# Performance work log

Hardware: AMD Instinct MI355X
Metric: run time of the kernel (lower is better)

The kernel has to match this reference:

```python
import jax, jax.numpy as jnp
import numpy as np
import math

ALPHA, BETA = 0.0, 0.1  # MarketRelation defaults


def setup_inputs() -> dict:
    key = jax.random.key(0)
    ks = jax.random.split(key, 15)
    n, T, d, K, C = 1024, 8, 64, 8, 64
    h = d  # hidden = (2*infeat)//2 = infeat
    s = 0.1
    u = jax.random.uniform(ks[13], (n, n, K), jnp.float32, 1e-6, 1.0 - 1e-6)
    return {
        "x":   jax.random.normal(ks[0], (n, T, d), jnp.float32),
        "Ind": jax.random.uniform(ks[1], (n, n), jnp.float32),
        "Loc": jax.random.uniform(ks[2], (n, n), jnp.float32),
        "a":   jax.random.normal(ks[3], (T, 1), jnp.float32),
        "W1m": jax.random.normal(ks[4], (2 * d, h), jnp.float32) * s,
        "b1m": jax.random.normal(ks[5], (h,), jnp.float32) * s,
        "W2m": jax.random.normal(ks[6], (h, 1), jnp.float32) * s,
        "b2m": jax.random.normal(ks[7], (1,), jnp.float32) * s,
        "W1s": jax.random.normal(ks[8], (2 * d, h), jnp.float32) * s,
        "b1s": jax.random.normal(ks[9], (h,), jnp.float32) * s,
        "W2s": jax.random.normal(ks[10], (h, K), jnp.float32) * s,
        "b2s": jax.random.normal(ks[11], (K,), jnp.float32) * s,
        "E":   jax.random.normal(ks[12], (K, n, C), jnp.float32) * s,
        "g":   -jnp.log(-jnp.log(u)),  # Gumbel(0,1) noise for gumbel_softmax
    }


def reference(x, Ind, Loc, a, W1m, b1m, W2m, b2m, W1s, b1s, W2s, b2s, E, g):
    n, T, d = x.shape
    # --- MarketRelation ---
    # fc1(concat(x_j, x_k)) == x_j @ W1m[:d] + x_k @ W1m[d:] + b1m (same math,
    # avoids materializing the N x N x 2d concat tensor)
    W1a, W1b = W1m[:d], W1m[d:]
    a_soft = jax.nn.softmax(a, axis=0)  # [T,1]
    A_mkt = jnp.zeros((n, n), x.dtype)
    for i in range(T):
        xi = x[:, i, :]                      # [n,d]
        hA = xi @ W1a                        # [n,h]
        hB = xi @ W1b                        # [n,h]
        hmat = jax.nn.relu(hA[:, None, :] + hB[None, :, :] + b1m)  # [n,n,h]
        adj = jax.nn.relu(hmat @ W2m + b2m)[..., 0]                # [n,n]
        factor = 1.0 + ALPHA * math.exp(-BETA * (T - i - 1))
        A_mkt = A_mkt + adj * (a_soft[i, 0] * factor)
    # --- NobsRelation (on last timestep) ---
    xl = x[:, -1, :]
    Ws1a, Ws1b = W1s[:d], W1s[d:]
    hs = jax.nn.relu((xl @ Ws1a)[:, None, :] + (xl @ Ws1b)[None, :, :] + b1s)
    logits = jax.nn.relu(hs @ W2s + b2s)          # [n,n,K]
    y = jax.nn.softmax(logits + g, axis=-1)       # gumbel_softmax, tau=1, soft
    D = jnp.einsum('knc,kmc->nmk', E, E)          # stack of E_k E_k^T, [n,n,K]
    A_nobs = jnp.sum(D * y, axis=-1)              # [n,n]
    return jnp.stack([Ind, Loc, A_mkt, A_nobs])   # [4,n,n]
```

## Files before the change

kernel.cpp:

```cpp
#include <hip/hip_runtime.h>

typedef unsigned short USH;
typedef float v2f __attribute__((ext_vector_type(2)));

__device__ __forceinline__ float bf2f(USH u) {
    return __uint_as_float(((unsigned int)u) << 16);
}
__device__ __forceinline__ float lo16(unsigned int u) { return __uint_as_float(u << 16); }
__device__ __forceinline__ float hi16(unsigned int u) { return __uint_as_float(u & 0xFFFF0000u); }
__device__ __forceinline__ USH f2bf(float f) {
    unsigned int i = __float_as_uint(f);
    i += 0x7FFFu + ((i >> 16) & 1u);
    return (USH)(i >> 16);
}
__device__ __forceinline__ v2f relu2(v2f s) {
    return __builtin_elementwise_max(s, (v2f)(0.0f));
}

__device__ __forceinline__ float ldf(const void* p, long idx, int bf) {
    return bf ? bf2f(((const USH*)p)[idx]) : ((const float*)p)[idx];
}
__device__ __forceinline__ void ld4(const void* p, long idx, int bf, float o[4]) {
    if (bf) {
        ushort4 u = *(const ushort4*)((const USH*)p + idx);
        o[0] = bf2f(u.x); o[1] = bf2f(u.y); o[2] = bf2f(u.z); o[3] = bf2f(u.w);
    } else {
        float4 v = *(const float4*)((const float*)p + idx);
        o[0] = v.x; o[1] = v.y; o[2] = v.z; o[3] = v.w;
    }
}

__device__ __forceinline__ int detect_bf(const void* ind) {
    const uint4* p = (const uint4*)ind;
    unsigned o = 0;
    #pragma unroll
    for (int i = 0; i < 8; ++i) { uint4 v = p[i]; o |= v.x | v.y | v.z | v.w; }
    return (o & 0x8000u) == 0;
}

__global__ __launch_bounds__(256) void k_pre_d(
    const void* __restrict__ x,
    const void* __restrict__ W1m,
    const void* __restrict__ b1m,
    const void* __restrict__ W1s,
    const void* __restrict__ b1s,
    const void* __restrict__ E,
    const void* __restrict__ IndDet,
    USH* __restrict__ hA, USH* __restrict__ hBb,
    USH* __restrict__ hsA, USH* __restrict__ hsBb,
    USH* __restrict__ D)
{
    __shared__ float smem[8192];
    float* sA = smem;
    float* sB = smem + 4096;
    const int bf = detect_bf(IndDet);
    const int tid = threadIdx.x;
    const int bid = blockIdx.x;
    const int tx = tid & 15, ty = tid >> 4;

    if (bid < 2048) {
        const int mb = (bid & 15) * 64, nb = ((bid >> 4) & 15) * 64, k = bid >> 8;
        const long ek = (long)k * 65536;
        {
            const int r_l = tid >> 2, cq = tid & 3;
            const long bn = ek + (long)(nb + r_l) * 64 + cq * 16;
            const long bm = ek + (long)(mb + r_l) * 64 + cq * 16;
            #pragma unroll
            for (int j = 0; j < 4; ++j) {
                const int c0 = cq * 16 + j * 4;
                float o[4];
                ld4(E, bn + j * 4, bf, o);
                #pragma unroll
                for (int e = 0; e < 4; ++e) sA[(c0 + e) * 64 + r_l] = o[e];
                ld4(E, bm + j * 4, bf, o);
                #pragma unroll
                for (int e = 0; e < 4; ++e) sB[(c0 + e) * 64 + r_l] = o[e];
            }
        }
        __syncthreads();
        const int m0 = tx * 4, n0 = ty * 4;
        float acc[4][4] = {};
        #pragma unroll 8
        for (int c = 0; c < 64; ++c) {
            const float4 an = *(const float4*)&sA[c * 64 + n0];
            const float4 am = *(const float4*)&sB[c * 64 + m0];
            const float aa[4] = {an.x, an.y, an.z, an.w};
            const float bb[4] = {am.x, am.y, am.z, am.w};
            #pragma unroll
            for (int ni = 0; ni < 4; ++ni)
                #pragma unroll
                for (int mi = 0; mi < 4; ++mi)
                    acc[ni][mi] += aa[ni] * bb[mi];
        }
        #pragma unroll
        for (int ni = 0; ni < 4; ++ni) {
            ushort4 o;
            o.x = f2bf(acc[ni][0]); o.y = f2bf(acc[ni][1]);
            o.z = f2bf(acc[ni][2]); o.w = f2bf(acc[ni][3]);
            *(ushort4*)&D[(long)k * 1048576 + (long)(nb + n0 + ni) * 1024 + mb + m0] = o;
        }
    } else {
        const int bid2 = bid - 2048;
        const int nbase = (bid2 & 15) * 64;
        const int by = bid2 >> 4;
        int t, rb;
        const void* Wsrc;
        const void* bias;
        USH* dst;
        if (by < 8)        { t = by;     rb = 0;  Wsrc = W1m; bias = nullptr; dst = hA + by * 65536; }
        else if (by < 16)  { t = by - 8; rb = 64; Wsrc = W1m; bias = b1m;     dst = hBb + (by - 8) * 65536; }
        else if (by == 16) { t = 7;      rb = 0;  Wsrc = W1s; bias = nullptr; dst = hsA; }
        else               { t = 7;      rb = 64; Wsrc = W1s; bias = b1s;     dst = hsBb; }

        {
            const int n_l = tid >> 2, dq = tid & 3;
            const long base = (long)(nbase + n_l) * 512 + t * 64 + dq * 16;
            #pragma unroll
            for (int j = 0; j < 4; ++j) {
                float o[4]; ld4(x, base + j * 4, bf, o);
                const int d0 = dq * 16 + j * 4;
                #pragma unroll
                for (int e = 0; e < 4; ++e) sA[(d0 + e) * 64 + n_l] = o[e];
            }
        }
        {
            const int d_l = tid >> 2, cq = tid & 3;
            const long base = (long)(rb + d_l) * 64 + cq * 16;
            #pragma unroll
            for (int j = 0; j < 4; ++j) {
                float o[4]; ld4(Wsrc, base + j * 4, bf, o);
                const int c0 = cq * 16 + j * 4;
                #pragma unroll
                for (int e = 0; e < 4; ++e) sB[d_l * 64 + c0 + e] = o[e];
            }
        }
        __syncthreads();

        const int c0 = tx * 4, nq = ty * 4;
        float acc[4][4] = {};
        #pragma unroll 16
        for (int d = 0; d < 64; ++d) {
            const float4 xa = *(const float4*)&sA[d * 64 + nq];
            const float4 wv = *(const float4*)&sB[d * 64 + c0];
            const float aa[4] = {xa.x, xa.y, xa.z, xa.w};
            const float ww[4] = {wv.x, wv.y, wv.z, wv.w};
            #pragma unroll
            for (int ci = 0; ci < 4; ++ci)
                #pragma unroll
                for (int ni = 0; ni < 4; ++ni)
                    acc[ci][ni] += ww[ci] * aa[ni];
        }
        #pragma unroll
        for (int ci = 0; ci < 4; ++ci) {
            const float bb = bias ? ldf(bias, c0 + ci, bf) : 0.0f;
            ushort4 o;
            o.x = f2bf(acc[ci][0] + bb); o.y = f2bf(acc[ci][1] + bb);
            o.z = f2bf(acc[ci][2] + bb); o.w = f2bf(acc[ci][3] + bb);
            *(ushort4*)&dst[(c0 + ci) * 1024 + nbase + nq] = o;
        }
    }
}

__global__ __launch_bounds__(256, 4) void k_main(
    const USH* __restrict__ hA, const USH* __restrict__ hBb,
    const USH* __restrict__ hsA, const USH* __restrict__ hsBb,
    const USH* __restrict__ Dm,
    const void* __restrict__ Ind, const void* __restrict__ Loc,
    const void* __restrict__ a, const void* __restrict__ W2m,
    const void* __restrict__ b2m, const void* __restrict__ W2s,
    const void* __restrict__ b2s, const void* __restrict__ g,
    void* __restrict__ out)
{
    __shared__ float As[2][64 * 32];
    __shared__ float Bs[2][64 * 32];
    __shared__ float w2s_l[64 * 8];
    __shared__ float w2m_l[64];
    __shared__ float asoft_l[8];

    const int bf = detect_bf(Ind);
    const int tid = threadIdx.x;
    const int mb = blockIdx.x * 32, nb = blockIdx.y * 32;
    const int tx = tid & 15, ty = tid >> 4;
    const int m0 = tx * 2, n0 = ty * 2;

    if (tid < 64) w2m_l[tid] = ldf(W2m, tid, bf);
    if (tid >= 64 && tid < 192) {
        const int q = tid - 64;
        float o[4]; ld4(W2s, q * 4, bf, o);
        #pragma unroll
        for (int e = 0; e < 4; ++e) w2s_l[q * 4 + e] = o[e];
    }
    if (tid < 8) {
        float av[8], mx = -1e30f, s = 0.0f;
        #pragma unroll
        for (int k = 0; k < 8; ++k) { av[k] = ldf(a, k, bf); mx = fmaxf(mx, av[k]); }
        #pragma unroll
        for (int k = 0; k < 8; ++k) s += __expf(av[k] - mx);
        asoft_l[tid] = __expf(av[tid] - mx) / s;
    }
    const float b2m_f = ldf(b2m, 0, bf);

    const int offA = (tid >> 2) * 1024 + nb + (tid & 3) * 8;
    const int offB = (tid >> 2) * 1024 + mb + (tid & 3) * 8;
    const int ldsOff = tid * 8;

    {
        const uint4 pa = *(const uint4*)(hA + offA);
        const uint4 pb = *(const uint4*)(hBb + offB);
        float4 fa0, fa1, fb0, fb1;
        fa0.x = lo16(pa.x); fa0.y = hi16(pa.x); fa0.z = lo16(pa.y); fa0.w = hi16(pa.y);
        fa1.x = lo16(pa.z); fa1.y = hi16(pa.z); fa1.z = lo16(pa.w); fa1.w = hi16(pa.w);
        fb0.x = lo16(pb.x); fb0.y = hi16(pb.x); fb0.z = lo16(pb.y); fb0.w = hi16(pb.y);
        fb1.x = lo16(pb.z); fb1.y = hi16(pb.z); fb1.z = lo16(pb.w); fb1.w = hi16(pb.w);
        *(float4*)&As[0][ldsOff] = fa0; *(float4*)&As[0][ldsOff + 4] = fa1;
        *(float4*)&Bs[0][ldsOff] = fb0; *(float4*)&Bs[0][ldsOff + 4] = fb1;
    }
    __syncthreads();

    v2f amk2[2] = {(v2f)(0.0f), (v2f)(0.0f)};

    for (int t = 0; t < 8; ++t) {
        const int cur = t & 1, nxt = cur ^ 1;
        const USH* srcA = (t < 7) ? (hA + (t + 1) * 65536) : hsA;
        const USH* srcB = (t < 7) ? (hBb + (t + 1) * 65536) : hsBb;
        const uint4 pa = *(const uint4*)(srcA + offA);
        const uint4 pb = *(const uint4*)(srcB + offB);

        v2f acc2[2] = {(v2f)(0.0f), (v2f)(0.0f)};
        #pragma unroll
        for (int c4 = 0; c4 < 16; ++c4) {
            const float4 wq = *(const float4*)&w2m_l[c4 * 4];
            const float ww[4] = {wq.x, wq.y, wq.z, wq.w};
            #pragma unroll
            for (int j = 0; j < 4; ++j) {
                const int c = c4 * 4 + j;
                const v2f aa = *(const v2f*)&As[cur][(c << 5) + n0];
                const v2f bb = *(const v2f*)&Bs[cur][(c << 5) + m0];
                const v2f wv = (v2f)(ww[j]);
                const v2f s0 = relu2((v2f)(aa.x) + bb);
                const v2f s1 = relu2((v2f)(aa.y) + bb);
                acc2[0] = __builtin_elementwise_fma(s0, wv, acc2[0]);
                acc2[1] = __builtin_elementwise_fma(s1, wv, acc2[1]);
            }
        }
        const v2f asv = (v2f)(asoft_l[t]);
        const v2f b2v = (v2f)(b2m_f);
        amk2[0] = __builtin_elementwise_fma(relu2(acc2[0] + b2v), asv, amk2[0]);
        amk2[1] = __builtin_elementwise_fma(relu2(acc2[1] + b2v), asv, amk2[1]);

        float4 f0, f1;
        f0.x = lo16(pa.x); f0.y = hi16(pa.x); f0.z = lo16(pa.y); f0.w = hi16(pa.y);
        f1.x = lo16(pa.z); f1.y = hi16(pa.z); f1.z = lo16(pa.w); f1.w = hi16(pa.w);
        *(float4*)&As[nxt][ldsOff] = f0; *(float4*)&As[nxt][ldsOff + 4] = f1;
        f0.x = lo16(pb.x); f0.y = hi16(pb.x); f0.z = lo16(pb.y); f0.w = hi16(pb.y);
        f1.x = lo16(pb.z); f1.y = hi16(pb.z); f1.z = lo16(pb.w); f1.w = hi16(pb.w);
        *(float4*)&Bs[nxt][ldsOff] = f0; *(float4*)&Bs[nxt][ldsOff + 4] = f1;
        __syncthreads();
    }

    v2f lgp[2][8];
    #pragma unroll
    for (int i = 0; i < 2; ++i)
        #pragma unroll
        for (int k = 0; k < 8; ++k) lgp[i][k] = (v2f)(0.0f);

    #pragma unroll 4
    for (int c = 0; c < 64; ++c) {
        const v2f aa = *(const v2f*)&As[0][(c << 5) + n0];
        const v2f bb = *(const v2f*)&Bs[0][(c << 5) + m0];
        const v2f z0 = relu2((v2f)(aa.x) + bb);
        const v2f z1 = relu2((v2f)(aa.y) + bb);
        const float4 wa = *(const float4*)&w2s_l[c << 3];
        const float4 wb = *(const float4*)&w2s_l[(c << 3) + 4];
        const float wk[8] = {wa.x, wa.y, wa.z, wa.w, wb.x, wb.y, wb.z, wb.w};
        #pragma unroll
        for (int k = 0; k < 8; ++k) {
            const v2f wkv = (v2f)(wk[k]);
            lgp[0][k] = __builtin_elementwise_fma(z0, wkv, lgp[0][k]);
            lgp[1][k] = __builtin_elementwise_fma(z1, wkv, lgp[1][k]);
        }
    }

    float b2s_f[8];
    #pragma unroll
    for (int k = 0; k < 8; ++k) b2s_f[k] = ldf(b2s, k, bf);

    #pragma unroll
    for (int i = 0; i < 2; ++i) {
        const long rowoff = (long)(nb + n0 + i) * 1024 + mb + m0;
        float gv[16];
        ld4(g, rowoff * 8 + 0, bf, gv + 0);
        ld4(g, rowoff * 8 + 4, bf, gv + 4);
        ld4(g, rowoff * 8 + 8, bf, gv + 8);
        ld4(g, rowoff * 8 + 12, bf, gv + 12);

        float s0 = 0.0f, s1 = 0.0f, d0 = 0.0f, d1 = 0.0f;
        #pragma unroll
        for (int k = 0; k < 8; ++k) {
            const v2f lr = relu2(lgp[i][k] + (v2f)(b2s_f[k]));
            const float e0 = __expf(lr.x + gv[k]);
            const float e1 = __expf(lr.y + gv[8 + k]);
            s0 += e0; s1 += e1;
            const ushort2 dv = *(const ushort2*)&Dm[((long)k << 20) + rowoff];
            d0 += bf2f(dv.x) * e0;
            d1 += bf2f(dv.y) * e1;
        }

        if (bf) {
            USH* o = (USH*)out;
            *(ushort2*)&o[rowoff] = *(const ushort2*)&((const USH*)Ind)[rowoff];
            *(ushort2*)&o[1048576 + rowoff] = *(const ushort2*)&((const USH*)Loc)[rowoff];
            ushort2 o2; o2.x = f2bf(amk2[i].x); o2.y = f2bf(amk2[i].y);
            *(ushort2*)&o[2 * 1048576 + rowoff] = o2;
            ushort2 o3; o3.x = f2bf(d0 / s0); o3.y = f2bf(d1 / s1);
            *(ushort2*)&o[3 * 1048576 + rowoff] = o3;
        } else {
            float* o = (float*)out;
            *(float2*)&o[rowoff] = *(const float2*)&((const float*)Ind)[rowoff];
            *(float2*)&o[1048576 + rowoff] = *(const float2*)&((const float*)Loc)[rowoff];
            float2 o2; o2.x = amk2[i].x; o2.y = amk2[i].y;
            *(float2*)&o[2 * 1048576 + rowoff] = o2;
            float2 o3; o3.x = d0 / s0; o3.y = d1 / s1;
            *(float2*)&o[3 * 1048576 + rowoff] = o3;
        }
    }
}

extern "C" void kernel_launch(void* const* d_in, const int* in_sizes, int n_in,
                              void* d_out, int out_size, void* d_ws, size_t ws_size,
                              hipStream_t stream) {
    const void* x   = d_in[0];
    const void* Ind = d_in[1];
    const void* Loc = d_in[2];
    const void* a   = d_in[3];
    const void* W1m = d_in[4];
    const void* b1m = d_in[5];
    const void* W2m = d_in[6];
    const void* b2m = d_in[7];
    const void* W1s = d_in[8];
    const void* b1s = d_in[9];
    const void* W2s = d_in[10];
    const void* b2s = d_in[11];
    const void* E   = d_in[12];
    const void* g   = d_in[13];

    USH* ws   = (USH*)d_ws;
    USH* hA   = ws;
    USH* hBb  = hA + 524288;
    USH* hsA  = hBb + 524288;
    USH* hsBb = hsA + 65536;
    USH* Dm   = hsBb + 65536;

    k_pre_d<<<dim3(2336), 256, 0, stream>>>(x, W1m, b1m, W1s, b1s, E, Ind,
                                            hA, hBb, hsA, hsBb, Dm);
    k_main<<<dim3(32, 32), 256, 0, stream>>>(hA, hBb, hsA, hsBb, Dm,
                                             Ind, Loc, a, W2m, b2m, W2s, b2s,
                                             g, d_out);
}
```

Before: 187.1 us.

## Store hidden projections in fp32 and enlarge main-kernel tile to 64x32

The precompute kernel now writes the hA/hB/hsA/hsB projections as fp32 instead of bf16. This removes the bf16 unpack work in the main kernel and may change numerics slightly. The main kernel's n-tile doubles to 64 rows, so each thread computes 4x2 outputs and each B element loaded into LDS is reused more. In exchange it uses more LDS, more registers (launch bounds drop to 2 blocks per CU), a bigger workspace, and launches half as many blocks.

```diff
diff --git a/kernel.cpp b/kernel.cpp
--- a/kernel.cpp
+++ b/kernel.cpp
@@ -46,8 +46,8 @@
     const void* __restrict__ b1s,
     const void* __restrict__ E,
     const void* __restrict__ IndDet,
-    USH* __restrict__ hA, USH* __restrict__ hBb,
-    USH* __restrict__ hsA, USH* __restrict__ hsBb,
+    float* __restrict__ hA, float* __restrict__ hBb,
+    float* __restrict__ hsA, float* __restrict__ hsBb,
     USH* __restrict__ D)
 {
     __shared__ float smem[8192];
@@ -106,7 +106,7 @@
         int t, rb;
         const void* Wsrc;
         const void* bias;
-        USH* dst;
+        float* dst;
         if (by < 8)        { t = by;     rb = 0;  Wsrc = W1m; bias = nullptr; dst = hA + by * 65536; }
         else if (by < 16)  { t = by - 8; rb = 64; Wsrc = W1m; bias = b1m;     dst = hBb + (by - 8) * 65536; }
         else if (by == 16) { t = 7;      rb = 0;  Wsrc = W1s; bias = nullptr; dst = hsA; }
@@ -153,17 +153,17 @@
         #pragma unroll
         for (int ci = 0; ci < 4; ++ci) {
             const float bb = bias ? ldf(bias, c0 + ci, bf) : 0.0f;
-            ushort4 o;
-            o.x = f2bf(acc[ci][0] + bb); o.y = f2bf(acc[ci][1] + bb);
-            o.z = f2bf(acc[ci][2] + bb); o.w = f2bf(acc[ci][3] + bb);
-            *(ushort4*)&dst[(c0 + ci) * 1024 + nbase + nq] = o;
-        }
-    }
-}
-
-__global__ __launch_bounds__(256, 4) void k_main(
-    const USH* __restrict__ hA, const USH* __restrict__ hBb,
-    const USH* __restrict__ hsA, const USH* __restrict__ hsBb,
+            float4 v;
+            v.x = acc[ci][0] + bb; v.y = acc[ci][1] + bb;
+            v.z = acc[ci][2] + bb; v.w = acc[ci][3] + bb;
+            *(float4*)&dst[(c0 + ci) * 1024 + nbase + nq] = v;
+        }
+    }
+}
+
+__global__ __launch_bounds__(256, 2) void k_main(
+    const float* __restrict__ hA, const float* __restrict__ hBb,
+    const float* __restrict__ hsA, const float* __restrict__ hsBb,
     const USH* __restrict__ Dm,
     const void* __restrict__ Ind, const void* __restrict__ Loc,
     const void* __restrict__ a, const void* __restrict__ W2m,
@@ -171,7 +171,7 @@
     const void* __restrict__ b2s, const void* __restrict__ g,
     void* __restrict__ out)
 {
-    __shared__ float As[2][64 * 32];
+    __shared__ float As[2][64 * 64];
     __shared__ float Bs[2][64 * 32];
     __shared__ float w2s_l[64 * 8];
     __shared__ float w2m_l[64];
@@ -179,9 +179,9 @@
 
     const int bf = detect_bf(Ind);
     const int tid = threadIdx.x;
-    const int mb = blockIdx.x * 32, nb = blockIdx.y * 32;
+    const int mb = blockIdx.x * 32, nb = blockIdx.y * 64;
     const int tx = tid & 15, ty = tid >> 4;
-    const int m0 = tx * 2, n0 = ty * 2;
+    const int m0 = tx * 2, n0 = ty * 4;
 
     if (tid < 64) w2m_l[tid] = ldf(W2m, tid, bf);
     if (tid >= 64 && tid < 192) {
@@ -200,33 +200,39 @@
     }
     const float b2m_f = ldf(b2m, 0, bf);
 
-    const int offA = (tid >> 2) * 1024 + nb + (tid & 3) * 8;
-    const int offB = (tid >> 2) * 1024 + mb + (tid & 3) * 8;
-    const int ldsOff = tid * 8;
-
-    {
-        const uint4 pa = *(const uint4*)(hA + offA);
-        const uint4 pb = *(const uint4*)(hBb + offB);
-        float4 fa0, fa1, fb0, fb1;
-        fa0.x = lo16(pa.x); fa0.y = hi16(pa.x); fa0.z = lo16(pa.y); fa0.w = hi16(pa.y);
-        fa1.x = lo16(pa.z); fa1.y = hi16(pa.z); fa1.z = lo16(pa.w); fa1.w = hi16(pa.w);
-        fb0.x = lo16(pb.x); fb0.y = hi16(pb.x); fb0.z = lo16(pb.y); fb0.w = hi16(pb.y);
-        fb1.x = lo16(pb.z); fb1.y = hi16(pb.z); fb1.z = lo16(pb.w); fb1.w = hi16(pb.w);
-        *(float4*)&As[0][ldsOff] = fa0; *(float4*)&As[0][ldsOff + 4] = fa1;
-        *(float4*)&Bs[0][ldsOff] = fb0; *(float4*)&Bs[0][ldsOff + 4] = fb1;
-    }
+    int gA[4], gB[2];
+    #pragma unroll
+    for (int j = 0; j < 4; ++j) {
+        const int ch = tid + j * 256;
+        gA[j] = (ch >> 4) * 1024 + nb + (ch & 15) * 4;
+    }
+    #pragma unroll
+    for (int j = 0; j < 2; ++j) {
+        const int ch = tid + j * 256;
+        gB[j] = (ch >> 3) * 1024 + mb + (ch & 7) * 4;
+    }
+
+    #pragma unroll
+    for (int j = 0; j < 4; ++j)
+        *(float4*)&As[0][(tid + j * 256) * 4] = *(const float4*)&hA[gA[j]];
+    #pragma unroll
+    for (int j = 0; j < 2; ++j)
+        *(float4*)&Bs[0][(tid + j * 256) * 4] = *(const float4*)&hBb[gB[j]];
     __syncthreads();
 
-    v2f amk2[2] = {(v2f)(0.0f), (v2f)(0.0f)};
+    v2f amk2[4] = {(v2f)(0.0f), (v2f)(0.0f), (v2f)(0.0f), (v2f)(0.0f)};
 
     for (int t = 0; t < 8; ++t) {
         const int cur = t & 1, nxt = cur ^ 1;
-        const USH* srcA = (t < 7) ? (hA + (t + 1) * 65536) : hsA;
-        const USH* srcB = (t < 7) ? (hBb + (t + 1) * 65536) : hsBb;
-        const uint4 pa = *(const uint4*)(srcA + offA);
-        const uint4 pb = *(const uint4*)(srcB + offB);
-
-        v2f acc2[2] = {(v2f)(0.0f), (v2f)(0.0f)};
+        const float* srcA = (t < 7) ? (hA + (t + 1) * 65536) : hsA;
+        const float* srcB = (t < 7) ? (hBb + (t + 1) * 65536) : hsBb;
+        float4 pa[4], pb[2];
+        #pragma unroll
+        for (int j = 0; j < 4; ++j) pa[j] = *(const float4*)&srcA[gA[j]];
+        #pragma unroll
+        for (int j = 0; j < 2; ++j) pb[j] = *(const float4*)&srcB[gB[j]];
+
+        v2f acc2[4] = {(v2f)(0.0f), (v2f)(0.0f), (v2f)(0.0f), (v2f)(0.0f)};
         #pragma unroll
         for (int c4 = 0; c4 < 16; ++c4) {
             const float4 wq = *(const float4*)&w2m_l[c4 * 4];
@@ -234,50 +240,55 @@
             #pragma unroll
             for (int j = 0; j < 4; ++j) {
                 const int c = c4 * 4 + j;
-                const v2f aa = *(const v2f*)&As[cur][(c << 5) + n0];
+                const float4 aa = *(const float4*)&As[cur][(c << 6) + n0];
                 const v2f bb = *(const v2f*)&Bs[cur][(c << 5) + m0];
                 const v2f wv = (v2f)(ww[j]);
-                const v2f s0 = relu2((v2f)(aa.x) + bb);
-                const v2f s1 = relu2((v2f)(aa.y) + bb);
-                acc2[0] = __builtin_elementwise_fma(s0, wv, acc2[0]);
-                acc2[1] = __builtin_elementwise_fma(s1, wv, acc2[1]);
+                const float an[4] = {aa.x, aa.y, aa.z, aa.w};
+                #pragma unroll
+                for (int i = 0; i < 4; ++i) {
+                    const v2f s = relu2((v2f)(an[i]) + bb);
+                    acc2[i] = __builtin_elementwise_fma(s, wv, acc2[i]);
+                }
             }
         }
         const v2f asv = (v2f)(asoft_l[t]);
         const v2f b2v = (v2f)(b2m_f);
-        amk2[0] = __builtin_elementwise_fma(relu2(acc2[0] + b2v), asv, amk2[0]);
-        amk2[1] = __builtin_elementwise_fma(relu2(acc2[1] + b2v), asv, amk2[1]);
-
-        float4 f0, f1;
-        f0.x = lo16(pa.x); f0.y = hi16(pa.x); f0.z = lo16(pa.y); f0.w = hi16(pa.y);
-        f1.x = lo16(pa.z); f1.y = hi16(pa.z); f1.z = lo16(pa.w); f1.w = hi16(pa.w);
-        *(float4*)&As[nxt][ldsOff] = f0; *(float4*)&As[nxt][ldsOff + 4] = f1;
-        f0.x = lo16(pb.x); f0.y = hi16(pb.x); f0.z = lo16(pb.y); f0.w = hi16(pb.y);
-        f1.x = lo16(pb.z); f1.y = hi16(pb.z); f1.z = lo16(pb.w); f1.w = hi16(pb.w);
-        *(float4*)&Bs[nxt][ldsOff] = f0; *(float4*)&Bs[nxt][ldsOff + 4] = f1;
+        #pragma unroll
+        for (int i = 0; i < 4; ++i)
+            amk2[i] = __builtin_elementwise_fma(relu2(acc2[i] + b2v), asv, amk2[i]);
+
+        #pragma unroll
+        for (int j = 0; j < 4; ++j)
+            *(float4*)&As[nxt][(tid + j * 256) * 4] = pa[j];
+        #pragma unroll
+        for (int j = 0; j < 2; ++j)
+            *(float4*)&Bs[nxt][(tid + j * 256) * 4] = pb[j];
         __syncthreads();
     }
 
-    v2f lgp[2][8];
-    #pragma unroll
-    for (int i = 0; i < 2; ++i)
+    v2f lgp[4][8];
+    #pragma unroll
+    for (int i = 0; i < 4; ++i)
         #pragma unroll
         for (int k = 0; k < 8; ++k) lgp[i][k] = (v2f)(0.0f);
 
     #pragma unroll 4
     for (int c = 0; c < 64; ++c) {
-        const v2f aa = *(const v2f*)&As[0][(c << 5) + n0];
+        const float4 aa = *(const float4*)&As[0][(c << 6) + n0];
         const v2f bb = *(const v2f*)&Bs[0][(c << 5) + m0];
-        const v2f z0 = relu2((v2f)(aa.x) + bb);
-        const v2f z1 = relu2((v2f)(aa.y) + bb);
+        const float an[4] = {aa.x, aa.y, aa.z, aa.w};
+        v2f z[4];
+        #pragma unroll
+        for (int i = 0; i < 4; ++i) z[i] = relu2((v2f)(an[i]) + bb);
         const float4 wa = *(const float4*)&w2s_l[c << 3];
         const float4 wb = *(const float4*)&w2s_l[(c << 3) + 4];
         const float wk[8] = {wa.x, wa.y, wa.z, wa.w, wb.x, wb.y, wb.z, wb.w};
         #pragma unroll
         for (int k = 0; k < 8; ++k) {
             const v2f wkv = (v2f)(wk[k]);
-            lgp[0][k] = __builtin_elementwise_fma(z0, wkv, lgp[0][k]);
-            lgp[1][k] = __builtin_elementwise_fma(z1, wkv, lgp[1][k]);
+            #pragma unroll
+            for (int i = 0; i < 4; ++i)
+                lgp[i][k] = __builtin_elementwise_fma(z[i], wkv, lgp[i][k]);
         }
     }
 
@@ -286,7 +297,7 @@
     for (int k = 0; k < 8; ++k) b2s_f[k] = ldf(b2s, k, bf);
 
     #pragma unroll
-    for (int i = 0; i < 2; ++i) {
+    for (int i = 0; i < 4; ++i) {
         const long rowoff = (long)(nb + n0 + i) * 1024 + mb + m0;
         float gv[16];
         ld4(g, rowoff * 8 + 0, bf, gv + 0);
@@ -344,16 +355,15 @@
     const void* E   = d_in[12];
     const void* g   = d_in[13];
 
-    USH* ws   = (USH*)d_ws;
-    USH* hA   = ws;
-    USH* hBb  = hA + 524288;
-    USH* hsA  = hBb + 524288;
-    USH* hsBb = hsA + 65536;
-    USH* Dm   = hsBb + 65536;
+    float* hAf   = (float*)d_ws;
+    float* hBbf  = hAf + 524288;
+    float* hsAf  = hBbf + 524288;
+    float* hsBbf = hsAf + 65536;
+    USH* Dm      = (USH*)(hsBbf + 65536);
 
     k_pre_d<<<dim3(2336), 256, 0, stream>>>(x, W1m, b1m, W1s, b1s, E, Ind,
-                                            hA, hBb, hsA, hsBb, Dm);
-    k_main<<<dim3(32, 32), 256, 0, stream>>>(hA, hBb, hsA, hsBb, Dm,
+                                            hAf, hBbf, hsAf, hsBbf, Dm);
+    k_main<<<dim3(32, 16), 256, 0, stream>>>(hAf, hBbf, hsAf, hsBbf, Dm,
                                              Ind, Loc, a, W2m, b2m, W2s, b2s,
                                              g, d_out);
 }
```

Result: slower. 202.8 us (+8.4%).

## Use bf16 MFMA for E·Eᵀ and enlarge main tile to 64x32 with 512 threads

Applied to the files above, without the earlier changes.

The D = E_k E_kᵀ precompute now uses bf16 16x16x32 MFMA instructions that read fragments directly from global memory, replacing the LDS-staged scalar FP32 outer-product loop. The aim is to cut the ALU and LDS cost of that 2048-block phase. Separately, the main kernel's tile grows to 64 rows by 32 columns with 512 threads and half as many blocks. This lets each B-tile load serve more outputs and lowers per-block setup overhead. In exchange, precision drops from FP32 accumulate-over-FP32 inputs to bf16 inputs when E is FP32, and occupancy may fall with larger blocks. D stores also become scalar 16-bit writes.

```diff
diff --git a/kernel.cpp b/kernel.cpp
--- a/kernel.cpp
+++ b/kernel.cpp
@@ -2,6 +2,8 @@
 
 typedef unsigned short USH;
 typedef float v2f __attribute__((ext_vector_type(2)));
+typedef float f32x4 __attribute__((ext_vector_type(4)));
+typedef __bf16 bf16x8 __attribute__((ext_vector_type(8)));
 
 __device__ __forceinline__ float bf2f(USH u) {
     return __uint_as_float(((unsigned int)u) << 16);
@@ -30,6 +32,15 @@
     }
 }
 
+__device__ __forceinline__ bf16x8 ld_bf8(const void* p, long idx, int bf) {
+    if (bf) return *(const bf16x8*)((const USH*)p + idx);
+    union { USH u[8]; bf16x8 v; } r;
+    const float* f = (const float*)p + idx;
+    #pragma unroll
+    for (int e = 0; e < 8; ++e) r.u[e] = f2bf(f[e]);
+    return r.v;
+}
+
 __device__ __forceinline__ int detect_bf(const void* ind) {
     const uint4* p = (const uint4*)ind;
     unsigned o = 0;
@@ -37,6 +48,7 @@
     for (int i = 0; i < 8; ++i) { uint4 v = p[i]; o |= v.x | v.y | v.z | v.w; }
     return (o & 0x8000u) == 0;
 }
+
 
 __global__ __launch_bounds__(256) void k_pre_d(
     const void* __restrict__ x,
@@ -56,50 +68,39 @@
     const int bf = detect_bf(IndDet);
     const int tid = threadIdx.x;
     const int bid = blockIdx.x;
-    const int tx = tid & 15, ty = tid >> 4;
 
     if (bid < 2048) {
         const int mb = (bid & 15) * 64, nb = ((bid >> 4) & 15) * 64, k = bid >> 8;
         const long ek = (long)k * 65536;
-        {
-            const int r_l = tid >> 2, cq = tid & 3;
-            const long bn = ek + (long)(nb + r_l) * 64 + cq * 16;
-            const long bm = ek + (long)(mb + r_l) * 64 + cq * 16;
-            #pragma unroll
-            for (int j = 0; j < 4; ++j) {
-                const int c0 = cq * 16 + j * 4;
-                float o[4];
-                ld4(E, bn + j * 4, bf, o);
-                #pragma unroll
-                for (int e = 0; e < 4; ++e) sA[(c0 + e) * 64 + r_l] = o[e];
-                ld4(E, bm + j * 4, bf, o);
-                #pragma unroll
-                for (int e = 0; e < 4; ++e) sB[(c0 + e) * 64 + r_l] = o[e];
+        const int lane = tid & 63, w = tid >> 6;
+        const int quad = lane >> 4, l15 = lane & 15;
+
+        const long arow = ek + (long)(nb + w * 16 + l15) * 64 + quad * 8;
+        bf16x8 afr0 = ld_bf8(E, arow, bf);
+        bf16x8 afr1 = ld_bf8(E, arow + 32, bf);
+
+        f32x4 acc[4];
+        #pragma unroll
+        for (int s = 0; s < 4; ++s) {
+            const long brow = ek + (long)(mb + s * 16 + l15) * 64 + quad * 8;
+            bf16x8 bfr0 = ld_bf8(E, brow, bf);
+            bf16x8 bfr1 = ld_bf8(E, brow + 32, bf);
+            f32x4 a = {0.0f, 0.0f, 0.0f, 0.0f};
+            a = __builtin_amdgcn_mfma_f32_16x16x32_bf16(afr0, bfr0, a, 0, 0, 0);
+            a = __builtin_amdgcn_mfma_f32_16x16x32_bf16(afr1, bfr1, a, 0, 0, 0);
+            acc[s] = a;
+        }
+        #pragma unroll
+        for (int s = 0; s < 4; ++s) {
+            #pragma unroll
+            for (int r = 0; r < 4; ++r) {
+                const int row = nb + w * 16 + quad * 4 + r;
+                D[(long)k * 1048576 + (long)row * 1024 + mb + s * 16 + l15] =
+                    f2bf(acc[s][r]);
             }
         }
-        __syncthreads();
-        const int m0 = tx * 4, n0 = ty * 4;
-        float acc[4][4] = {};
-        #pragma unroll 8
-        for (int c = 0; c < 64; ++c) {
-            const float4 an = *(const float4*)&sA[c * 64 + n0];
-            const float4 am = *(const float4*)&sB[c * 64 + m0];
-            const float aa[4] = {an.x, an.y, an.z, an.w};
-            const float bb[4] = {am.x, am.y, am.z, am.w};
-            #pragma unroll
-            for (int ni = 0; ni < 4; ++ni)
-                #pragma unroll
-                for (int mi = 0; mi < 4; ++mi)
-                    acc[ni][mi] += aa[ni] * bb[mi];
-        }
-        #pragma unroll
-        for (int ni = 0; ni < 4; ++ni) {
-            ushort4 o;
-            o.x = f2bf(acc[ni][0]); o.y = f2bf(acc[ni][1]);
-            o.z = f2bf(acc[ni][2]); o.w = f2bf(acc[ni][3]);
-            *(ushort4*)&D[(long)k * 1048576 + (long)(nb + n0 + ni) * 1024 + mb + m0] = o;
-        }
     } else {
+        const int tx = tid & 15, ty = tid >> 4;
         const int bid2 = bid - 2048;
         const int nbase = (bid2 & 15) * 64;
         const int by = bid2 >> 4;
@@ -161,7 +162,7 @@
     }
 }
 
-__global__ __launch_bounds__(256, 4) void k_main(
+__global__ __launch_bounds__(512, 4) void k_main(
     const USH* __restrict__ hA, const USH* __restrict__ hBb,
     const USH* __restrict__ hsA, const USH* __restrict__ hsBb,
     const USH* __restrict__ Dm,
@@ -171,7 +172,7 @@
     const void* __restrict__ b2s, const void* __restrict__ g,
     void* __restrict__ out)
 {
-    __shared__ float As[2][64 * 32];
+    __shared__ float As[2][64 * 64];
     __shared__ float Bs[2][64 * 32];
     __shared__ float w2s_l[64 * 8];
     __shared__ float w2m_l[64];
@@ -179,7 +180,7 @@
 
     const int bf = detect_bf(Ind);
     const int tid = threadIdx.x;
-    const int mb = blockIdx.x * 32, nb = blockIdx.y * 32;
+    const int mb = blockIdx.x * 32, nb = blockIdx.y * 64;
     const int tx = tid & 15, ty = tid >> 4;
     const int m0 = tx * 2, n0 = ty * 2;
 
@@ -200,20 +201,20 @@
     }
     const float b2m_f = ldf(b2m, 0, bf);
 
-    const int offA = (tid >> 2) * 1024 + nb + (tid & 3) * 8;
-    const int offB = (tid >> 2) * 1024 + mb + (tid & 3) * 8;
-    const int ldsOff = tid * 8;
+    const int offA = (tid >> 3) * 1024 + nb + (tid & 7) * 8;
+    const int offB = (tid >> 3) * 1024 + mb + (tid & 7) * 4;
+    const int ldsA = tid * 8, ldsB = tid * 4;
 
     {
         const uint4 pa = *(const uint4*)(hA + offA);
-        const uint4 pb = *(const uint4*)(hBb + offB);
-        float4 fa0, fa1, fb0, fb1;
-        fa0.x = lo16(pa.x); fa0.y = hi16(pa.x); fa0.z = lo16(pa.y); fa0.w = hi16(pa.y);
-        fa1.x = lo16(pa.z); fa1.y = hi16(pa.z); fa1.z = lo16(pa.w); fa1.w = hi16(pa.w);
-        fb0.x = lo16(pb.x); fb0.y = hi16(pb.x); fb0.z = lo16(pb.y); fb0.w = hi16(pb.y);
-        fb1.x = lo16(pb.z); fb1.y = hi16(pb.z); fb1.z = lo16(pb.w); fb1.w = hi16(pb.w);
-        *(float4*)&As[0][ldsOff] = fa0; *(float4*)&As[0][ldsOff + 4] = fa1;
-        *(float4*)&Bs[0][ldsOff] = fb0; *(float4*)&Bs[0][ldsOff + 4] = fb1;
+        const uint2 pb = *(const uint2*)(hBb + offB);
+        float4 f0, f1;
+        f0.x = lo16(pa.x); f0.y = hi16(pa.x); f0.z = lo16(pa.y); f0.w = hi16(pa.y);
+        f1.x = lo16(pa.z); f1.y = hi16(pa.z); f1.z = lo16(pa.w); f1.w = hi16(pa.w);
+        *(float4*)&As[0][ldsA] = f0; *(float4*)&As[0][ldsA + 4] = f1;
+        float4 fb;
+        fb.x = lo16(pb.x); fb.y = hi16(pb.x); fb.z = lo16(pb.y); fb.w = hi16(pb.y);
+        *(float4*)&Bs[0][ldsB] = fb;
     }
     __syncthreads();
 
@@ -224,7 +225,7 @@
         const USH* srcA = (t < 7) ? (hA + (t + 1) * 65536) : hsA;
         const USH* srcB = (t < 7) ? (hBb + (t + 1) * 65536) : hsBb;
         const uint4 pa = *(const uint4*)(srcA + offA);
-        const uint4 pb = *(const uint4*)(srcB + offB);
+        const uint2 pb = *(const uint2*)(srcB + offB);
 
         v2f acc2[2] = {(v2f)(0.0f), (v2f)(0.0f)};
         #pragma unroll
@@ -234,7 +235,7 @@
             #pragma unroll
             for (int j = 0; j < 4; ++j) {
                 const int c = c4 * 4 + j;
-                const v2f aa = *(const v2f*)&As[cur][(c << 5) + n0];
+                const v2f aa = *(const v2f*)&As[cur][(c << 6) + n0];
                 const v2f bb = *(const v2f*)&Bs[cur][(c << 5) + m0];
                 const v2f wv = (v2f)(ww[j]);
                 const v2f s0 = relu2((v2f)(aa.x) + bb);
@@ -251,10 +252,10 @@
         float4 f0, f1;
         f0.x = lo16(pa.x); f0.y = hi16(pa.x); f0.z = lo16(pa.y); f0.w = hi16(pa.y);
         f1.x = lo16(pa.z); f1.y = hi16(pa.z); f1.z = lo16(pa.w); f1.w = hi16(pa.w);
-        *(float4*)&As[nxt][ldsOff] = f0; *(float4*)&As[nxt][ldsOff + 4] = f1;
-        f0.x = lo16(pb.x); f0.y = hi16(pb.x); f0.z = lo16(pb.y); f0.w = hi16(pb.y);
-        f1.x = lo16(pb.z); f1.y = hi16(pb.z); f1.z = lo16(pb.w); f1.w = hi16(pb.w);
-        *(float4*)&Bs[nxt][ldsOff] = f0; *(float4*)&Bs[nxt][ldsOff + 4] = f1;
+        *(float4*)&As[nxt][ldsA] = f0; *(float4*)&As[nxt][ldsA + 4] = f1;
+        float4 fb;
+        fb.x = lo16(pb.x); fb.y = hi16(pb.x); fb.z = lo16(pb.y); fb.w = hi16(pb.y);
+        *(float4*)&Bs[nxt][ldsB] = fb;
         __syncthreads();
     }
 
@@ -266,7 +267,7 @@
 
     #pragma unroll 4
     for (int c = 0; c < 64; ++c) {
-        const v2f aa = *(const v2f*)&As[0][(c << 5) + n0];
+        const v2f aa = *(const v2f*)&As[0][(c << 6) + n0];
         const v2f bb = *(const v2f*)&Bs[0][(c << 5) + m0];
         const v2f z0 = relu2((v2f)(aa.x) + bb);
         const v2f z1 = relu2((v2f)(aa.y) + bb);
@@ -353,7 +354,7 @@
 
     k_pre_d<<<dim3(2336), 256, 0, stream>>>(x, W1m, b1m, W1s, b1s, E, Ind,
                                             hA, hBb, hsA, hsBb, Dm);
-    k_main<<<dim3(32, 32), 256, 0, stream>>>(hA, hBb, hsA, hsBb, Dm,
+    k_main<<<dim3(32, 16), 512, 0, stream>>>(hA, hBb, hsA, hsBb, Dm,
                                              Ind, Loc, a, W2m, b2m, W2s, b2s,
                                              g, d_out);
 }
```

Measured after the change: 189.5 us. No clear change (+1.3%).
